# Kernel tuning notes

Hardware: AMD Instinct MI355X
Metric: run time of the kernel (lower is better)

## Reference

```python
import jax, jax.numpy as jnp
import numpy as np
from jax import lax

# ---- static config (matches init_kwargs) ----
B, D, H, HD, MLP = 64, 768, 12, 64, 3072
DEPTH = 11                     # trunk blocks; block 12 is used (twice) as b1/b2
IMG_H, IMG_W, P, S = 256, 128, 16, 12
NY, NX = (IMG_H - P) // S + 1, (IMG_W - P) // S + 1   # 21, 10
NP = NY * NX                   # 210 patches
N = NP + 1                     # +CLS = 211 tokens
NUM_CIDS = 8
SCALE = HD ** -0.5
SIE = 3.0                      # sie_xishu
SHIFT, GROUPS, DIV = 5, 2, 4
EPS = 1e-6
_PNAMES = ["ln1_g", "ln1_b", "qkv_w", "qkv_b", "proj_w", "proj_b",
           "ln2_g", "ln2_b", "fc1_w", "fc1_b", "fc2_w", "fc2_b"]


def layernorm(x, g, b):
    m = jnp.mean(x, -1, keepdims=True)
    v = jnp.mean(jnp.square(x - m), -1, keepdims=True)
    return (x - m) * lax.rsqrt(v + EPS) * g + b


def block(x, p):
    """Pre-norm ViT block: manual attention (q@k.T softmax @v) + GELU MLP."""
    ln1g, ln1b, qkvw, qkvb, projw, projb, ln2g, ln2b, fc1w, fc1b, fc2w, fc2b = p
    Bn, Nn = x.shape[0], x.shape[1]
    h = layernorm(x, ln1g, ln1b)
    qkv = (h @ qkvw + qkvb).reshape(Bn, Nn, 3, H, HD)
    q, k, v = qkv[:, :, 0], qkv[:, :, 1], qkv[:, :, 2]           # [B,N,H,HD]
    attn = jax.nn.softmax(jnp.einsum('bnhd,bmhd->bhnm', q * SCALE, k), axis=-1)
    o = jnp.einsum('bhnm,bmhd->bnhd', attn, v).reshape(Bn, Nn, D)
    x = x + o @ projw + projb
    h = layernorm(x, ln2g, ln2b)
    return x + jax.nn.gelu(h @ fc1w + fc1b, approximate=False) @ fc2w + fc2b


def _block_params(k, lead=()):
    ks = jax.random.split(k, 4)
    z = lambda s: jnp.zeros(lead + s, jnp.float32)
    o = lambda s: jnp.ones(lead + s, jnp.float32)
    r = lambda kk, s, fan: jax.random.normal(kk, lead + s, jnp.float32) * (fan ** -0.5)
    return dict(ln1_g=o((D,)), ln1_b=z((D,)),
                qkv_w=r(ks[0], (D, 3 * D), D), qkv_b=z((3 * D,)),
                proj_w=r(ks[1], (D, D), D), proj_b=z((D,)),
                ln2_g=o((D,)), ln2_b=z((D,)),
                fc1_w=r(ks[2], (D, MLP), D), fc1_b=z((MLP,)),
                fc2_w=r(ks[3], (MLP, D), MLP), fc2_b=z((D,)))


def setup_inputs() -> dict:
    key = jax.random.key(0)
    k = jax.random.split(key, 8)
    inp = {
        "x": jax.random.normal(k[0], (B, 3, IMG_H, IMG_W), jnp.float32),
        "cids": jax.random.randint(k[1], (B,), 0, NUM_CIDS),
        "conv_w": jax.random.normal(k[2], (D, 3, P, P), jnp.float32) * np.float32(np.sqrt(2.0 / (P * P * D))),
        "conv_b": jnp.zeros((D,), jnp.float32),
        "cls_token": jax.random.normal(k[3], (1, 1, D), jnp.float32) * 0.02,
        "pos_embed": jax.random.normal(k[4], (1, N, D), jnp.float32) * 0.02,
        "sie_embed": jax.random.normal(k[5], (NUM_CIDS, 1, D), jnp.float32) * 0.02,
    }
    for name, arr in _block_params(k[6], (DEPTH,)).items():
        inp["blk_" + name] = arr
    for pre, kk in (("b1_", jax.random.fold_in(key, 101)), ("b2_", jax.random.fold_in(key, 102))):
        for name, arr in _block_params(kk).items():
            inp[pre + name] = arr
        inp[pre + "norm_g"] = jnp.ones((D,), jnp.float32)
        inp[pre + "norm_b"] = jnp.zeros((D,), jnp.float32)
    return inp


def reference(x, cids, conv_w, conv_b, cls_token, pos_embed, sie_embed,
              blk_ln1_g, blk_ln1_b, blk_qkv_w, blk_qkv_b, blk_proj_w, blk_proj_b,
              blk_ln2_g, blk_ln2_b, blk_fc1_w, blk_fc1_b, blk_fc2_w, blk_fc2_b,
              b1_ln1_g, b1_ln1_b, b1_qkv_w, b1_qkv_b, b1_proj_w, b1_proj_b,
              b1_ln2_g, b1_ln2_b, b1_fc1_w, b1_fc1_b, b1_fc2_w, b1_fc2_b,
              b1_norm_g, b1_norm_b,
              b2_ln1_g, b2_ln1_b, b2_qkv_w, b2_qkv_b, b2_proj_w, b2_proj_b,
              b2_ln2_g, b2_ln2_b, b2_fc1_w, b2_fc1_b, b2_fc2_w, b2_fc2_b,
              b2_norm_g, b2_norm_b):
    Bn = x.shape[0]
    # overlapping patch embed: Conv2d(3->768, k=16, s=12), flatten, transpose
    y = lax.conv_general_dilated(x, conv_w, (S, S), 'VALID',
                                 dimension_numbers=('NCHW', 'OIHW', 'NCHW'))
    y = (y + conv_b[None, :, None, None]).reshape(Bn, D, NP).transpose(0, 2, 1)
    t = jnp.concatenate([jnp.broadcast_to(cls_token, (Bn, 1, D)), y], axis=1)
    t = t + pos_embed + SIE * sie_embed[cids]   # SIE camera embedding
    # 11 trunk blocks via scan over stacked params
    stk = (blk_ln1_g, blk_ln1_b, blk_qkv_w, blk_qkv_b, blk_proj_w, blk_proj_b,
           blk_ln2_g, blk_ln2_b, blk_fc1_w, blk_fc1_b, blk_fc2_w, blk_fc2_b)
    t = lax.scan(lambda c, p: (block(c, p), None), t, stk)[0]
    # global branch: b1 = block12 + final norm, take CLS
    b1p = (b1_ln1_g, b1_ln1_b, b1_qkv_w, b1_qkv_b, b1_proj_w, b1_proj_b,
           b1_ln2_g, b1_ln2_b, b1_fc1_w, b1_fc1_b, b1_fc2_w, b1_fc2_b)
    f0 = layernorm(block(t, b1p), b1_norm_g, b1_norm_b)[:, 0]
    # shuffle_unit(t, shift=5, group=2, begin=1) -> jigsaw rearranged patches [B,210,D]
    xs = jnp.concatenate([t[:, SHIFT:], t[:, 1:SHIFT]], axis=1)
    xs = xs.reshape(Bn, GROUPS, -1, D).transpose(0, 2, 1, 3).reshape(Bn, -1, D)
    token = t[:, 0:1]
    pl = NP // DIV                                   # 52
    b2p = (b2_ln1_g, b2_ln1_b, b2_qkv_w, b2_qkv_b, b2_proj_w, b2_proj_b,
           b2_ln2_g, b2_ln2_b, b2_fc1_w, b2_fc1_b, b2_fc2_w, b2_fc2_b)
    feats = [f0]
    for i in range(DIV):
        seg = jnp.concatenate([token, xs[:, i * pl:(i + 1) * pl]], axis=1)   # [B,53,D]
        feats.append(layernorm(block(seg, b2p), b2_norm_g, b2_norm_b)[:, 0])
    # eval output with neck_feat='before': necks pass features through;
    # concat global + local/divide_length -> [B, 5*768]
    return jnp.concatenate([feats[0]] + [f / DIV for f in feats[1:]], axis=1)
```

## Files before the change

kernel.cpp:

```cpp
#include <hip/hip_runtime.h>
#include <hip/hip_bf16.h>
#include <cstdint>
#include <cstddef>
#include <math.h>

using bf16 = __hip_bfloat16;
typedef __bf16 bf16x8 __attribute__((ext_vector_type(8)));
typedef float f32x4 __attribute__((ext_vector_type(4)));

static constexpr int NHEAD = 12;
static constexpr int NTOK  = 211;
static constexpr int DEPTH = 11;

static __device__ __forceinline__ void gload_lds16(const bf16* g, bf16* lds) {
  __builtin_amdgcn_global_load_lds(
      (const __attribute__((address_space(1))) uint32_t*)g,
      (__attribute__((address_space(3))) uint32_t*)lds,
      16, 0, 0);
}

__device__ __forceinline__ float gelu_f(float x) {
  float u = x * (0.7978845608f + 0.0356774081f * x * x);
  float t = 1.f - 2.f / (__expf(2.f * u) + 1.f);
  return 0.5f * x * (1.f + t);
}

static __device__ __forceinline__ unsigned short bf16_bits(float x) {
  return __builtin_bit_cast(unsigned short, __float2bfloat16(x));
}

template <bool GELU, bool RES, typename CT>
__global__ __launch_bounds__(256) void gemm_db(
    const bf16* __restrict__ A, const bf16* __restrict__ Bt,
    const float* __restrict__ bias, const float* __restrict__ res,
    CT* __restrict__ C, int M, int N, int K, int gn, int sA, int sR, int sC)
{
  __shared__ bf16 sb[2][8192];

  const int tid = threadIdx.x;
  const int w = tid >> 6, l = tid & 63;
  const int lr = l & 15, lg = l >> 4;
  const int wr = (w >> 1) * 64, wc = (w & 1) * 64;

  const int nwg = gridDim.x, lin = blockIdx.x;
  const int q = nwg >> 3, r = nwg & 7;
  const int xcd = lin & 7, pos = lin >> 3;
  const int wg = (xcd < r ? xcd * (q + 1) : r * (q + 1) + (xcd - r) * q) + pos;
  const int bm0 = (wg / gn) * 128, bn0 = (wg % gn) * 128;

  f32x4 acc[4][4];
#pragma unroll
  for (int i = 0; i < 4; ++i)
#pragma unroll
    for (int j = 0; j < 4; ++j) acc[i][j] = f32x4{0.f, 0.f, 0.f, 0.f};

  size_t aof[2], bof[2]; int dst[2];
#pragma unroll
  for (int j = 0; j < 2; ++j) {
    const int c = j * 256 + tid;
    const int row = c >> 2;
    const int ch = (c & 3) ^ ((row >> 1) & 3);
    int ar = bm0 + row; if (ar >= M) ar = M - 1;
    aof[j] = (size_t)ar * sA + ch * 8;
    bof[j] = (size_t)(bn0 + row) * K + ch * 8;
    dst[j] = c * 8;
  }

  const int nt = K >> 5;

  auto stage = [&](int t) {
    bf16* s = sb[t & 1];
    const size_t ko = (size_t)t * 32;
    gload_lds16(A + aof[0] + ko, s + dst[0]);
    gload_lds16(A + aof[1] + ko, s + dst[1]);
    gload_lds16(Bt + bof[0] + ko, s + 4096 + dst[0]);
    gload_lds16(Bt + bof[1] + ko, s + 4096 + dst[1]);
  };

  stage(0);
  __syncthreads();

  const int swz = (lg ^ ((lr >> 1) & 3)) * 8;

  for (int t = 0; t < nt; ++t) {
    if (t + 1 < nt) stage(t + 1);
    const bf16* As = sb[t & 1];
    const bf16* Bs = As + 4096;
    bf16x8 af[4], bv[4];
#pragma unroll
    for (int mi = 0; mi < 4; ++mi)
      af[mi] = *(const bf16x8*)(As + (wr + mi * 16 + lr) * 32 + swz);
#pragma unroll
    for (int ni = 0; ni < 4; ++ni)
      bv[ni] = *(const bf16x8*)(Bs + (wc + ni * 16 + lr) * 32 + swz);
#pragma unroll
    for (int mi = 0; mi < 4; ++mi)
#pragma unroll
      for (int ni = 0; ni < 4; ++ni)
        acc[mi][ni] = __builtin_amdgcn_mfma_f32_16x16x32_bf16(af[mi], bv[ni], acc[mi][ni], 0, 0, 0);
    __syncthreads();
  }

  if constexpr (sizeof(CT) == 2) {
    char* lb = (char*)sb;
#pragma unroll
    for (int mi = 0; mi < 4; ++mi) {
#pragma unroll
      for (int ni = 0; ni < 4; ++ni) {
        const int cloc = wc + ni * 16 + lr;
        const float bvl = bias[bn0 + cloc];
#pragma unroll
        for (int r2 = 0; r2 < 4; ++r2) {
          const int rowl = wr + mi * 16 + lg * 4 + r2;
          float v = acc[mi][ni][r2] + bvl;
          if constexpr (GELU) v = gelu_f(v);
          *(unsigned short*)(lb + rowl * 256 + ((cloc * 2) ^ (((rowl >> 1) & 6) << 4))) =
              bf16_bits(v);
        }
      }
    }
    __syncthreads();
#pragma unroll
    for (int j = 0; j < 8; ++j) {
      const int flat = j * 256 + tid;
      const int row = flat >> 4, ch = flat & 15;
      const int grow = bm0 + row;
      if (grow < M) {
        const f32x4 v = *(const f32x4*)(lb + row * 256 + ((ch * 16) ^ (((row >> 1) & 6) << 4)));
        *(f32x4*)((char*)C + ((size_t)grow * sC + bn0 + ch * 8) * 2) = v;
      }
    }
  } else {
#pragma unroll
    for (int mi = 0; mi < 4; ++mi) {
#pragma unroll
      for (int ni = 0; ni < 4; ++ni) {
        const int col = bn0 + wc + ni * 16 + lr;
        const float bvl = bias[col];
#pragma unroll
        for (int r2 = 0; r2 < 4; ++r2) {
          const int row = bm0 + wr + mi * 16 + lg * 4 + r2;
          if (row < M) {
            float v = acc[mi][ni][r2] + bvl;
            if constexpr (GELU) v = gelu_f(v);
            if constexpr (RES) v += res[(size_t)row * sR + col];
            C[(size_t)row * sC + col] = v;
          }
        }
      }
    }
  }
}

__global__ __launch_bounds__(256) void vtrans_kernel(
    const bf16* __restrict__ qkv, bf16* __restrict__ vT, int ntok, int pad)
{
  __shared__ unsigned short t[224 * 65];
  const int bb = blockIdx.x, h = blockIdx.y;
  const unsigned short* src = (const unsigned short*)qkv + (size_t)bb * ntok * 2304 + 1536 + h * 64;
  for (int idx = threadIdx.x; idx < ntok * 64; idx += 256) {
    int tok = idx >> 6, d = idx & 63;
    t[tok * 65 + d] = src[(size_t)tok * 2304 + d];
  }
  __syncthreads();
  unsigned short* dst = (unsigned short*)vT + (size_t)(bb * 12 + h) * 64 * pad;
  for (int idx = threadIdx.x; idx < 64 * ntok; idx += 256) {
    int d = idx / ntok, tok = idx - d * ntok;
    dst[(size_t)d * pad + tok] = t[tok * 65 + d];
  }
}

template <int NKF, bool ONLY0>
__global__ __launch_bounds__(256) void attn_kernel(
    const bf16* __restrict__ qkv, const bf16* __restrict__ vT,
    bf16* __restrict__ ao, int ntok, int pad)
{
  constexpr int NPAD = NKF * 16;
  __shared__ bf16 Pl[4][16][NPAD];
  const int bb = blockIdx.x;
  const int h = blockIdx.y;
  const int tid = threadIdx.x;
  const int w = tid >> 6, l = tid & 63;
  const int lr = l & 15, lg = l >> 4;
  if (ONLY0 && w > 0) return;
  const __bf16* base = reinterpret_cast<const __bf16*>(qkv) + (size_t)bb * ntok * 2304 + h * 64;
  const __bf16* vt = reinterpret_cast<const __bf16*>(vT) + (size_t)(bb * 12 + h) * 64 * pad;

  for (int qt = w; qt < (ONLY0 ? 1 : NKF); qt += 4) {
    int qrow = qt * 16 + lr; if (qrow >= ntok) qrow = ntok - 1;
    const __bf16* qp = base + (size_t)qrow * 2304 + lg * 8;
    const bf16x8 qf0 = *reinterpret_cast<const bf16x8*>(qp);
    const bf16x8 qf1 = *reinterpret_cast<const bf16x8*>(qp + 32);

    f32x4 s[NKF];
#pragma unroll
    for (int kf = 0; kf < NKF; ++kf) {
      int krow = kf * 16 + lr; if (krow >= ntok) krow = ntok - 1;
      const __bf16* kp = base + (size_t)krow * 2304 + 768 + lg * 8;
      f32x4 a = f32x4{0.f, 0.f, 0.f, 0.f};
      a = __builtin_amdgcn_mfma_f32_16x16x32_bf16(qf0, *reinterpret_cast<const bf16x8*>(kp), a, 0, 0, 0);
      a = __builtin_amdgcn_mfma_f32_16x16x32_bf16(qf1, *reinterpret_cast<const bf16x8*>(kp + 32), a, 0, 0, 0);
      s[kf] = a;
    }

    float rs[4];
#pragma unroll
    for (int r = 0; r < 4; ++r) {
      float mx = -1e30f;
#pragma unroll
      for (int kf = 0; kf < NKF; ++kf)
        if (kf * 16 + lr < ntok) mx = fmaxf(mx, s[kf][r]);
#pragma unroll
      for (int d = 1; d < 16; d <<= 1) mx = fmaxf(mx, __shfl_xor(mx, d));
      float sum = 0.f;
#pragma unroll
      for (int kf = 0; kf < NKF; ++kf) {
        float p = 0.f;
        if (kf * 16 + lr < ntok) p = __expf((s[kf][r] - mx) * 0.125f);
        sum += p;
        Pl[w][lg * 4 + r][kf * 16 + lr] = __float2bfloat16(p);
      }
#pragma unroll
      for (int d = 1; d < 16; d <<= 1) sum += __shfl_xor(sum, d);
      rs[r] = sum;
    }
    __builtin_amdgcn_s_waitcnt(0);

    f32x4 o[4];
#pragma unroll
    for (int ni = 0; ni < 4; ++ni) o[ni] = f32x4{0.f, 0.f, 0.f, 0.f};
#pragma unroll
    for (int ks = 0; ks < NPAD / 32; ++ks) {
      const bf16x8 pa = *reinterpret_cast<const bf16x8*>(&Pl[w][lr][ks * 32 + lg * 8]);
#pragma unroll
      for (int ni = 0; ni < 4; ++ni) {
        const bf16x8 vb = *reinterpret_cast<const bf16x8*>(
            vt + (size_t)(ni * 16 + lr) * pad + ks * 32 + lg * 8);
        o[ni] = __builtin_amdgcn_mfma_f32_16x16x32_bf16(pa, vb, o[ni], 0, 0, 0);
      }
    }
#pragma unroll
    for (int ni = 0; ni < 4; ++ni)
#pragma unroll
      for (int r = 0; r < 4; ++r) {
        int qq = qt * 16 + lg * 4 + r;
        if (qq < (ONLY0 ? 1 : ntok)) {
          float val = o[ni][r] / rs[r];
          ao[((size_t)bb * ntok + qq) * 768 + h * 64 + ni * 16 + lr] = __float2bfloat16(val);
        }
      }
  }
}

static __device__ __forceinline__ void ln_row(
    const float* __restrict__ x, const float* __restrict__ g, const float* __restrict__ b,
    bf16* __restrict__ out, int row, int l)
{
  const float4* xr = reinterpret_cast<const float4*>(x + (size_t)row * 768);
  float4 v[3]; float s = 0.f;
#pragma unroll
  for (int i = 0; i < 3; ++i) {
    v[i] = xr[l + i * 64];
    s += v[i].x + v[i].y + v[i].z + v[i].w;
  }
#pragma unroll
  for (int d = 1; d < 64; d <<= 1) s += __shfl_xor(s, d);
  float mean = s * (1.f / 768.f);
  float s2 = 0.f;
#pragma unroll
  for (int i = 0; i < 3; ++i) {
    float a0 = v[i].x - mean, a1 = v[i].y - mean, a2 = v[i].z - mean, a3 = v[i].w - mean;
    s2 += a0 * a0 + a1 * a1 + a2 * a2 + a3 * a3;
  }
#pragma unroll
  for (int d = 1; d < 64; d <<= 1) s2 += __shfl_xor(s2, d);
  float rstd = rsqrtf(s2 * (1.f / 768.f) + 1e-6f);
  const float4* g4 = reinterpret_cast<const float4*>(g);
  const float4* b4 = reinterpret_cast<const float4*>(b);
  unsigned short* orow = reinterpret_cast<unsigned short*>(out + (size_t)row * 768);
#pragma unroll
  for (int i = 0; i < 3; ++i) {
    float4 gg = g4[l + i * 64], bb = b4[l + i * 64];
    ushort4 pk;
    pk.x = bf16_bits((v[i].x - mean) * rstd * gg.x + bb.x);
    pk.y = bf16_bits((v[i].y - mean) * rstd * gg.y + bb.y);
    pk.z = bf16_bits((v[i].z - mean) * rstd * gg.z + bb.z);
    pk.w = bf16_bits((v[i].w - mean) * rstd * gg.w + bb.w);
    *reinterpret_cast<ushort4*>(orow + (l + i * 64) * 4) = pk;
  }
}

__global__ __launch_bounds__(256) void ln_kernel(
    const float* __restrict__ x, const float* __restrict__ g, const float* __restrict__ b,
    bf16* __restrict__ out, int Mrows)
{
  int row = blockIdx.x * 4 + (threadIdx.x >> 6);
  if (row >= Mrows) return;
  ln_row(x, g, b, out, row, threadIdx.x & 63);
}

__global__ __launch_bounds__(256) void tln_kernel(
    const float* __restrict__ w0, const float* __restrict__ w1,
    const float* __restrict__ w2, const float* __restrict__ w3,
    bf16* __restrict__ d0, bf16* __restrict__ d1,
    bf16* __restrict__ d2, bf16* __restrict__ d3,
    const float* __restrict__ x, const float* __restrict__ g,
    const float* __restrict__ b, bf16* __restrict__ outh, int Mrows)
{
  __shared__ float tile[32][33];
  int id = blockIdx.x;
  if (id >= 6912) {
    int row = (id - 6912) * 4 + (threadIdx.x >> 6);
    if (row < Mrows) ln_row(x, g, b, outh, row, threadIdx.x & 63);
    return;
  }
  const float* in; bf16* out; int R, C, tt;
  if (id < 1728)      { in = w0; out = d0; R = 768;  C = 2304; tt = id; }
  else if (id < 2304) { in = w1; out = d1; R = 768;  C = 768;  tt = id - 1728; }
  else if (id < 4608) { in = w2; out = d2; R = 768;  C = 3072; tt = id - 2304; }
  else                { in = w3; out = d3; R = 3072; C = 768;  tt = id - 4608; }
  const int tc = C >> 5;
  int c0 = (tt % tc) * 32, r0 = (tt / tc) * 32;
  int tx = threadIdx.x & 31, ty = threadIdx.x >> 5;
#pragma unroll
  for (int i = 0; i < 4; ++i) {
    int rr = ty + i * 8;
    tile[rr][tx] = in[(size_t)(r0 + rr) * C + c0 + tx];
  }
  __syncthreads();
#pragma unroll
  for (int i = 0; i < 4; ++i) {
    int c = ty + i * 8;
    out[(size_t)(c0 + c) * R + r0 + tx] = __float2bfloat16(tile[tx][c]);
  }
}

__global__ __launch_bounds__(256) void ln_head_kernel(
    const float* __restrict__ x, int tokstride, const float* __restrict__ g,
    const float* __restrict__ b, float* __restrict__ out, int nbb, int mode)
{
  int bb = blockIdx.x * 4 + (threadIdx.x >> 6);
  if (bb >= nbb) return;
  int l = threadIdx.x & 63;
  const float* xr = x + (size_t)bb * tokstride * 768;
  float v[12]; float s = 0.f;
#pragma unroll
  for (int i = 0; i < 12; ++i) { v[i] = xr[l + i * 64]; s += v[i]; }
#pragma unroll
  for (int d = 1; d < 64; d <<= 1) s += __shfl_xor(s, d);
  float mean = s * (1.f / 768.f);
  float s2 = 0.f;
#pragma unroll
  for (int i = 0; i < 12; ++i) { float t = v[i] - mean; s2 += t * t; }
#pragma unroll
  for (int d = 1; d < 64; d <<= 1) s2 += __shfl_xor(s2, d);
  float rstd = rsqrtf(s2 * (1.f / 768.f) + 1e-6f);
  float scale = mode ? 0.25f : 1.f;
  int b_ = mode ? (bb & 63) : bb;
  int off = mode ? (1 + (bb >> 6)) * 768 : 0;
  float* orow = out + (size_t)b_ * 3840 + off;
#pragma unroll
  for (int i = 0; i < 12; ++i) {
    orow[l + i * 64] = ((v[i] - mean) * rstd * g[l + i * 64] + b[l + i * 64]) * scale;
  }
}

__global__ void prep_kernel(const float* __restrict__ x, bf16* __restrict__ pm,
                            const float* __restrict__ convw, bf16* __restrict__ cw)
{
  int idx = blockIdx.x * 256 + threadIdx.x;
  if (idx < 13440 * 768) {
    int k = idx % 768;
    int m = idx / 768;
    int b = m / 210, p = m % 210;
    int py = p / 10, px = p % 10;
    int c = k >> 8, ij = k & 255, i = ij >> 4, j = ij & 15;
    pm[idx] = __float2bfloat16(x[(((size_t)b * 3 + c) * 256 + py * 12 + i) * 128 + px * 12 + j]);
  } else {
    int idx2 = idx - 13440 * 768;
    if (idx2 < 768 * 768) cw[idx2] = __float2bfloat16(convw[idx2]);
  }
}

__global__ void assemble_kernel(
    const bf16* __restrict__ y, const float* __restrict__ cls, const float* __restrict__ pos,
    const float* __restrict__ sie, const int* __restrict__ cids, float* __restrict__ tA)
{
  int idx = blockIdx.x * 256 + threadIdx.x;
  if (idx >= 13504 * 768) return;
  int d = idx % 768;
  int t = (idx / 768) % 211;
  int b = idx / (768 * 211);
  float v = pos[t * 768 + d] + 3.0f * sie[cids[b] * 768 + d];
  if (t == 0) v += cls[d];
  else v += __bfloat162float(y[((size_t)b * 210 + (t - 1)) * 768 + d]);
  tA[idx] = v;
}

__global__ void gather_kernel(const float* __restrict__ tA, float* __restrict__ tB)
{
  int idx = blockIdx.x * 256 + threadIdx.x;
  if (idx >= 256 * 53 * 768) return;
  int d = idx % 768;
  int jj = (idx / 768) % 53;
  int bb = idx / (768 * 53);
  int i = bb >> 6, b = bb & 63;
  int src;
  if (jj == 0) src = 0;
  else {
    int jx = i * 52 + (jj - 1);
    int mm = (jx & 1) * 105 + (jx >> 1);
    src = (mm < 206) ? (5 + mm) : (1 + (mm - 206));
  }
  tB[idx] = tA[((size_t)b * 211 + src) * 768 + d];
}

struct BlkP {
  const float *ln1_g, *ln1_b, *qkv_w, *qkv_b, *proj_w, *proj_b;
  const float *ln2_g, *ln2_b, *fc1_w, *fc1_b, *fc2_w, *fc2_b;
};

extern "C" void kernel_launch(void* const* d_in, const int* in_sizes, int n_in,
                              void* d_out, int out_size, void* d_ws, size_t ws_size,
                              hipStream_t stream)
{
  (void)in_sizes; (void)n_in; (void)out_size; (void)ws_size;
  const float* xin   = (const float*)d_in[0];
  const int*   cids  = (const int*)  d_in[1];
  const float* convw = (const float*)d_in[2];
  const float* convb = (const float*)d_in[3];
  const float* cls   = (const float*)d_in[4];
  const float* pos   = (const float*)d_in[5];
  const float* sie   = (const float*)d_in[6];
  float* out = (float*)d_out;

  char* ws = (char*)d_ws;
  bf16*  qkvT = (bf16*)(ws + 0);
  bf16*  projT = (bf16*)(ws + 3538944);
  bf16*  fc1T = (bf16*)(ws + 4718592);
  bf16*  fc2T = (bf16*)(ws + 9437184);
  float* tA   = (float*)(ws + 14155776);
  float* tB   = (float*)(ws + 55640064);
  bf16*  hb   = (bf16*)(ws + 97320960);
  bf16*  big  = (bf16*)(ws + 118161408);
  bf16*  ao   = (bf16*)(ws + 201523200);
  bf16*  vTb  = (bf16*)(ws + 222363648);
  char*  sbuf = ws + 118161408 + 73400320;
  float* y0   = (float*)(sbuf);
  bf16*  hb0  = (bf16*)(sbuf + 786432);
  bf16*  big0 = (bf16*)(sbuf + 1179648);
  float* f0b  = (float*)(sbuf + 2752512);

  dim3 blk(256);

  auto apply_block = [&](float* xbuf, const BlkP& p, int nb, int ntok_) {
    const int M = nb * ntok_;
    const int gm = (M + 127) / 128;
    const int pad = (ntok_ == NTOK) ? 224 : 64;
    tln_kernel<<<dim3(6912 + (M + 3) / 4), blk, 0, stream>>>(
        p.qkv_w, p.proj_w, p.fc1_w, p.fc2_w, qkvT, projT, fc1T, fc2T,
        xbuf, p.ln1_g, p.ln1_b, hb, M);
    gemm_db<false, false, bf16><<<dim3(gm * 18), blk, 0, stream>>>(
        hb, qkvT, p.qkv_b, nullptr, big, M, 2304, 768, 18, 768, 2304, 2304);
    vtrans_kernel<<<dim3(nb, NHEAD), blk, 0, stream>>>(big, vTb, ntok_, pad);
    attn_kernel<14, false><<<dim3(nb, NHEAD), blk, 0, stream>>>(big, vTb, ao, ntok_, pad);
    gemm_db<false, true, float><<<dim3(gm * 6), blk, 0, stream>>>(
        ao, projT, p.proj_b, xbuf, xbuf, M, 768, 768, 6, 768, 768, 768);
    ln_kernel<<<dim3((M + 3) / 4), blk, 0, stream>>>(xbuf, p.ln2_g, p.ln2_b, hb, M);
    gemm_db<true, false, bf16><<<dim3(gm * 24), blk, 0, stream>>>(
        hb, fc1T, p.fc1_b, nullptr, big, M, 3072, 768, 24, 768, 3072, 3072);
    gemm_db<false, true, float><<<dim3(gm * 6), blk, 0, stream>>>(
        big, fc2T, p.fc2_b, xbuf, xbuf, M, 768, 3072, 6, 3072, 768, 768);
  };

  auto apply_head_block = [&](const float* xsrc, const BlkP& p, int nb, int ntok_,
                              const float* ng, const float* nbias, int mode) {
    const int M = nb * ntok_;
    const int gm = (M + 127) / 128;
    const int gm0 = (nb + 127) / 128;
    const int pad = (ntok_ == NTOK) ? 224 : 64;
    const int ts = ntok_ * 768;
    tln_kernel<<<dim3(6912 + (M + 3) / 4), blk, 0, stream>>>(
        p.qkv_w, p.proj_w, p.fc1_w, p.fc2_w, qkvT, projT, fc1T, fc2T,
        xsrc, p.ln1_g, p.ln1_b, hb, M);
    gemm_db<false, false, bf16><<<dim3(gm * 12), blk, 0, stream>>>(
        hb, qkvT + 768 * 768, p.qkv_b + 768, nullptr, big + 768,
        M, 1536, 768, 12, 768, 0, 2304);
    gemm_db<false, false, bf16><<<dim3(gm0 * 6), blk, 0, stream>>>(
        hb, qkvT, p.qkv_b, nullptr, big,
        nb, 768, 768, 6, ntok_ * 768, 0, ntok_ * 2304);
    vtrans_kernel<<<dim3(nb, NHEAD), blk, 0, stream>>>(big, vTb, ntok_, pad);
    if (ntok_ == NTOK)
      attn_kernel<14, true><<<dim3(nb, NHEAD), blk, 0, stream>>>(big, vTb, ao, ntok_, pad);
    else
      attn_kernel<4, true><<<dim3(nb, NHEAD), blk, 0, stream>>>(big, vTb, ao, ntok_, pad);
    gemm_db<false, true, float><<<dim3(gm0 * 6), blk, 0, stream>>>(
        ao, projT, p.proj_b, xsrc, y0, nb, 768, 768, 6, ts, ts, 768);
    ln_kernel<<<dim3((nb + 3) / 4), blk, 0, stream>>>(y0, p.ln2_g, p.ln2_b, hb0, nb);
    gemm_db<true, false, bf16><<<dim3(gm0 * 24), blk, 0, stream>>>(
        hb0, fc1T, p.fc1_b, nullptr, big0, nb, 3072, 768, 24, 768, 3072, 3072);
    gemm_db<false, true, float><<<dim3(gm0 * 6), blk, 0, stream>>>(
        big0, fc2T, p.fc2_b, y0, f0b, nb, 768, 3072, 6, 3072, 768, 768);
    ln_head_kernel<<<dim3((nb + 3) / 4), blk, 0, stream>>>(
        f0b, 1, ng, nbias, out, nb, mode);
  };

  {
    int total = 13440 * 768 + 768 * 768;
    prep_kernel<<<dim3((total + 255) / 256), blk, 0, stream>>>(xin, big, convw, qkvT);
    gemm_db<false, false, bf16><<<dim3(105 * 6), blk, 0, stream>>>(
        big, qkvT, convb, nullptr, ao, 13440, 768, 768, 6, 768, 768, 768);
    total = 13504 * 768;
    assemble_kernel<<<dim3((total + 255) / 256), blk, 0, stream>>>(ao, cls, pos, sie, cids, tA);
  }

  const float* bp[12];
  for (int i = 0; i < 12; ++i) bp[i] = (const float*)d_in[7 + i];
  for (int dd = 0; dd < DEPTH; ++dd) {
    BlkP p;
    p.ln1_g = bp[0] + dd * 768;                p.ln1_b = bp[1] + dd * 768;
    p.qkv_w = bp[2] + (size_t)dd * 768 * 2304; p.qkv_b = bp[3] + dd * 2304;
    p.proj_w = bp[4] + (size_t)dd * 768 * 768; p.proj_b = bp[5] + dd * 768;
    p.ln2_g = bp[6] + dd * 768;                p.ln2_b = bp[7] + dd * 768;
    p.fc1_w = bp[8] + (size_t)dd * 768 * 3072; p.fc1_b = bp[9] + dd * 3072;
    p.fc2_w = bp[10] + (size_t)dd * 3072 * 768; p.fc2_b = bp[11] + dd * 768;
    apply_block(tA, p, 64, NTOK);
  }

  {
    BlkP p;
    p.ln1_g = (const float*)d_in[19]; p.ln1_b = (const float*)d_in[20];
    p.qkv_w = (const float*)d_in[21]; p.qkv_b = (const float*)d_in[22];
    p.proj_w = (const float*)d_in[23]; p.proj_b = (const float*)d_in[24];
    p.ln2_g = (const float*)d_in[25]; p.ln2_b = (const float*)d_in[26];
    p.fc1_w = (const float*)d_in[27]; p.fc1_b = (const float*)d_in[28];
    p.fc2_w = (const float*)d_in[29]; p.fc2_b = (const float*)d_in[30];
    apply_head_block(tA, p, 64, NTOK,
                     (const float*)d_in[31], (const float*)d_in[32], 0);
  }

  {
    int total = 256 * 53 * 768;
    gather_kernel<<<dim3((total + 255) / 256), blk, 0, stream>>>(tA, tB);
    BlkP p;
    p.ln1_g = (const float*)d_in[33]; p.ln1_b = (const float*)d_in[34];
    p.qkv_w = (const float*)d_in[35]; p.qkv_b = (const float*)d_in[36];
    p.proj_w = (const float*)d_in[37]; p.proj_b = (const float*)d_in[38];
    p.ln2_g = (const float*)d_in[39]; p.ln2_b = (const float*)d_in[40];
    p.fc1_w = (const float*)d_in[41]; p.fc1_b = (const float*)d_in[42];
    p.fc2_w = (const float*)d_in[43]; p.fc2_b = (const float*)d_in[44];
    apply_head_block(tB, p, 256, 53,
                     (const float*)d_in[45], (const float*)d_in[46], 1);
  }
}
```

Before: 5.102 ms.

## Scatter QKV GEMM output into per-head contiguous Q/K/V buffers

The QKV GEMM epilogue now writes Q, K and V directly into head-major [batch*head, pad, 64] buffers instead of an interleaved [tokens, 2304] matrix. The attention kernel and the V-transpose kernel read these contiguous per-head tiles, which avoids strided 4.6KB-row gathers. The cost is extra index math in the epilogue and a rearranged workspace layout whose buffers may overlap.

Result: no change. 5.088 ms (-0.3%).

```diff
diff --git a/kernel.cpp b/kernel.cpp
--- a/kernel.cpp
+++ b/kernel.cpp
@@ -29,11 +29,13 @@
   return __builtin_bit_cast(unsigned short, __float2bfloat16(x));
 }
 
-template <bool GELU, bool RES, typename CT>
+template <bool GELU, bool RES, typename CT, int OUT>
 __global__ __launch_bounds__(256) void gemm_db(
     const bf16* __restrict__ A, const bf16* __restrict__ Bt,
     const float* __restrict__ bias, const float* __restrict__ res,
-    CT* __restrict__ C, int M, int N, int K, int gn, int sA, int sR, int sC)
+    CT* __restrict__ C, int M, int N, int K, int gn, int sA, int sR, int sC,
+    bf16* __restrict__ qh, bf16* __restrict__ kh, bf16* __restrict__ vh,
+    int pad, int ntd, int coff)
 {
   __shared__ bf16 sb[2][8192];
 
@@ -101,7 +103,7 @@
     __syncthreads();
   }
 
-  if constexpr (sizeof(CT) == 2) {
+  if constexpr (OUT == 2 || sizeof(CT) == 2) {
     char* lb = (char*)sb;
 #pragma unroll
     for (int mi = 0; mi < 4; ++mi) {
@@ -127,7 +129,18 @@
       const int grow = bm0 + row;
       if (grow < M) {
         const f32x4 v = *(const f32x4*)(lb + row * 256 + ((ch * 16) ^ (((row >> 1) & 6) << 4)));
-        *(f32x4*)((char*)C + ((size_t)grow * sC + bn0 + ch * 8) * 2) = v;
+        if constexpr (OUT == 2) {
+          const int col0 = bn0 + ch * 8 + coff;
+          const int region = (col0 >= 1536) ? 2 : (col0 >= 768 ? 1 : 0);
+          const int c7 = col0 - region * 768;
+          const int h = c7 >> 6, d = c7 & 63;
+          const int bb2 = grow / ntd;
+          const int tok = grow - bb2 * ntd;
+          bf16* db = (region == 0) ? qh : ((region == 1) ? kh : vh);
+          *(f32x4*)((char*)db + (((size_t)(bb2 * 12 + h) * pad + tok) * 64 + d) * 2) = v;
+        } else {
+          *(f32x4*)((char*)C + ((size_t)grow * sC + bn0 + ch * 8) * 2) = v;
+        }
       }
     }
   } else {
@@ -153,27 +166,27 @@
 }
 
 __global__ __launch_bounds__(256) void vtrans_kernel(
-    const bf16* __restrict__ qkv, bf16* __restrict__ vT, int ntok, int pad)
+    const bf16* __restrict__ vcomp, bf16* __restrict__ vT, int ntok, int pad)
 {
   __shared__ unsigned short t[224 * 65];
   const int bb = blockIdx.x, h = blockIdx.y;
-  const unsigned short* src = (const unsigned short*)qkv + (size_t)bb * ntok * 2304 + 1536 + h * 64;
+  const unsigned short* src = (const unsigned short*)vcomp + (size_t)(bb * 12 + h) * pad * 64;
   for (int idx = threadIdx.x; idx < ntok * 64; idx += 256) {
     int tok = idx >> 6, d = idx & 63;
-    t[tok * 65 + d] = src[(size_t)tok * 2304 + d];
+    t[tok * 65 + d] = src[idx];
   }
   __syncthreads();
-  unsigned short* dst = (unsigned short*)vT + (size_t)(bb * 12 + h) * 64 * pad;
+  unsigned short* dstp = (unsigned short*)vT + (size_t)(bb * 12 + h) * 64 * pad;
   for (int idx = threadIdx.x; idx < 64 * ntok; idx += 256) {
     int d = idx / ntok, tok = idx - d * ntok;
-    dst[(size_t)d * pad + tok] = t[tok * 65 + d];
+    dstp[(size_t)d * pad + tok] = t[tok * 65 + d];
   }
 }
 
 template <int NKF, bool ONLY0>
 __global__ __launch_bounds__(256) void attn_kernel(
-    const bf16* __restrict__ qkv, const bf16* __restrict__ vT,
-    bf16* __restrict__ ao, int ntok, int pad)
+    const bf16* __restrict__ qb, const bf16* __restrict__ kb,
+    const bf16* __restrict__ vT, bf16* __restrict__ ao, int ntok, int pad)
 {
   constexpr int NPAD = NKF * 16;
   __shared__ bf16 Pl[4][16][NPAD];
@@ -183,12 +196,14 @@
   const int w = tid >> 6, l = tid & 63;
   const int lr = l & 15, lg = l >> 4;
   if (ONLY0 && w > 0) return;
-  const __bf16* base = reinterpret_cast<const __bf16*>(qkv) + (size_t)bb * ntok * 2304 + h * 64;
-  const __bf16* vt = reinterpret_cast<const __bf16*>(vT) + (size_t)(bb * 12 + h) * 64 * pad;
+  const int bbh = bb * 12 + h;
+  const __bf16* qbase = reinterpret_cast<const __bf16*>(qb) + (size_t)bbh * pad * 64;
+  const __bf16* kbase = reinterpret_cast<const __bf16*>(kb) + (size_t)bbh * pad * 64;
+  const __bf16* vt = reinterpret_cast<const __bf16*>(vT) + (size_t)bbh * 64 * pad;
 
   for (int qt = w; qt < (ONLY0 ? 1 : NKF); qt += 4) {
     int qrow = qt * 16 + lr; if (qrow >= ntok) qrow = ntok - 1;
-    const __bf16* qp = base + (size_t)qrow * 2304 + lg * 8;
+    const __bf16* qp = qbase + qrow * 64 + lg * 8;
     const bf16x8 qf0 = *reinterpret_cast<const bf16x8*>(qp);
     const bf16x8 qf1 = *reinterpret_cast<const bf16x8*>(qp + 32);
 
@@ -196,7 +211,7 @@
 #pragma unroll
     for (int kf = 0; kf < NKF; ++kf) {
       int krow = kf * 16 + lr; if (krow >= ntok) krow = ntok - 1;
-      const __bf16* kp = base + (size_t)krow * 2304 + 768 + lg * 8;
+      const __bf16* kp = kbase + krow * 64 + lg * 8;
       f32x4 a = f32x4{0.f, 0.f, 0.f, 0.f};
       a = __builtin_amdgcn_mfma_f32_16x16x32_bf16(qf0, *reinterpret_cast<const bf16x8*>(kp), a, 0, 0, 0);
       a = __builtin_amdgcn_mfma_f32_16x16x32_bf16(qf1, *reinterpret_cast<const bf16x8*>(kp + 32), a, 0, 0, 0);
@@ -442,14 +457,17 @@
   float* tA   = (float*)(ws + 14155776);
   float* tB   = (float*)(ws + 55640064);
   bf16*  hb   = (bf16*)(ws + 97320960);
+  bf16*  qb   = (bf16*)(ws + 118161408);
+  bf16*  kb   = (bf16*)(ws + 143327232);
+  bf16*  vb   = (bf16*)(ws + 168493056);
   bf16*  big  = (bf16*)(ws + 118161408);
-  bf16*  ao   = (bf16*)(ws + 201523200);
-  bf16*  vTb  = (bf16*)(ws + 222363648);
-  char*  sbuf = ws + 118161408 + 73400320;
+  char*  sbuf = ws + 193658880;
   float* y0   = (float*)(sbuf);
   bf16*  hb0  = (bf16*)(sbuf + 786432);
   bf16*  big0 = (bf16*)(sbuf + 1179648);
   float* f0b  = (float*)(sbuf + 2752512);
+  bf16*  ao   = (bf16*)(ws + 201523200);
+  bf16*  vTb  = (bf16*)(ws + 222363648);
 
   dim3 blk(256);
 
@@ -460,17 +478,21 @@
     tln_kernel<<<dim3(6912 + (M + 3) / 4), blk, 0, stream>>>(
         p.qkv_w, p.proj_w, p.fc1_w, p.fc2_w, qkvT, projT, fc1T, fc2T,
         xbuf, p.ln1_g, p.ln1_b, hb, M);
-    gemm_db<false, false, bf16><<<dim3(gm * 18), blk, 0, stream>>>(
-        hb, qkvT, p.qkv_b, nullptr, big, M, 2304, 768, 18, 768, 2304, 2304);
-    vtrans_kernel<<<dim3(nb, NHEAD), blk, 0, stream>>>(big, vTb, ntok_, pad);
-    attn_kernel<14, false><<<dim3(nb, NHEAD), blk, 0, stream>>>(big, vTb, ao, ntok_, pad);
-    gemm_db<false, true, float><<<dim3(gm * 6), blk, 0, stream>>>(
-        ao, projT, p.proj_b, xbuf, xbuf, M, 768, 768, 6, 768, 768, 768);
+    gemm_db<false, false, bf16, 2><<<dim3(gm * 18), blk, 0, stream>>>(
+        hb, qkvT, p.qkv_b, nullptr, (bf16*)nullptr, M, 2304, 768, 18, 768, 0, 0,
+        qb, kb, vb, pad, ntok_, 0);
+    vtrans_kernel<<<dim3(nb, NHEAD), blk, 0, stream>>>(vb, vTb, ntok_, pad);
+    attn_kernel<14, false><<<dim3(nb, NHEAD), blk, 0, stream>>>(qb, kb, vTb, ao, ntok_, pad);
+    gemm_db<false, true, float, 0><<<dim3(gm * 6), blk, 0, stream>>>(
+        ao, projT, p.proj_b, xbuf, xbuf, M, 768, 768, 6, 768, 768, 768,
+        nullptr, nullptr, nullptr, 0, 1, 0);
     ln_kernel<<<dim3((M + 3) / 4), blk, 0, stream>>>(xbuf, p.ln2_g, p.ln2_b, hb, M);
-    gemm_db<true, false, bf16><<<dim3(gm * 24), blk, 0, stream>>>(
-        hb, fc1T, p.fc1_b, nullptr, big, M, 3072, 768, 24, 768, 3072, 3072);
-    gemm_db<false, true, float><<<dim3(gm * 6), blk, 0, stream>>>(
-        big, fc2T, p.fc2_b, xbuf, xbuf, M, 768, 3072, 6, 3072, 768, 768);
+    gemm_db<true, false, bf16, 0><<<dim3(gm * 24), blk, 0, stream>>>(
+        hb, fc1T, p.fc1_b, nullptr, big, M, 3072, 768, 24, 768, 3072, 3072,
+        nullptr, nullptr, nullptr, 0, 1, 0);
+    gemm_db<false, true, float, 0><<<dim3(gm * 6), blk, 0, stream>>>(
+        big, fc2T, p.fc2_b, xbuf, xbuf, M, 768, 3072, 6, 3072, 768, 768,
+        nullptr, nullptr, nullptr, 0, 1, 0);
   };
 
   auto apply_head_block = [&](const float* xsrc, const BlkP& p, int nb, int ntok_,
@@ -483,24 +505,27 @@
     tln_kernel<<<dim3(6912 + (M + 3) / 4), blk, 0, stream>>>(
         p.qkv_w, p.proj_w, p.fc1_w, p.fc2_w, qkvT, projT, fc1T, fc2T,
         xsrc, p.ln1_g, p.ln1_b, hb, M);
-    gemm_db<false, false, bf16><<<dim3(gm * 12), blk, 0, stream>>>(
-        hb, qkvT + 768 * 768, p.qkv_b + 768, nullptr, big + 768,
-        M, 1536, 768, 12, 768, 0, 2304);
-    gemm_db<false, false, bf16><<<dim3(gm0 * 6), blk, 0, stream>>>(
-        hb, qkvT, p.qkv_b, nullptr, big,
-        nb, 768, 768, 6, ntok_ * 768, 0, ntok_ * 2304);
-    vtrans_kernel<<<dim3(nb, NHEAD), blk, 0, stream>>>(big, vTb, ntok_, pad);
+    gemm_db<false, false, bf16, 2><<<dim3(gm * 12), blk, 0, stream>>>(
+        hb, qkvT + 768 * 768, p.qkv_b + 768, nullptr, (bf16*)nullptr,
+        M, 1536, 768, 12, 768, 0, 0, qb, kb, vb, pad, ntok_, 768);
+    gemm_db<false, false, bf16, 2><<<dim3(gm0 * 6), blk, 0, stream>>>(
+        hb, qkvT, p.qkv_b, nullptr, (bf16*)nullptr,
+        nb, 768, 768, 6, ntok_ * 768, 0, 0, qb, kb, vb, pad, 1, 0);
+    vtrans_kernel<<<dim3(nb, NHEAD), blk, 0, stream>>>(vb, vTb, ntok_, pad);
     if (ntok_ == NTOK)
-      attn_kernel<14, true><<<dim3(nb, NHEAD), blk, 0, stream>>>(big, vTb, ao, ntok_, pad);
+      attn_kernel<14, true><<<dim3(nb, NHEAD), blk, 0, stream>>>(qb, kb, vTb, ao, ntok_, pad);
     else
-      attn_kernel<4, true><<<dim3(nb, NHEAD), blk, 0, stream>>>(big, vTb, ao, ntok_, pad);
-    gemm_db<false, true, float><<<dim3(gm0 * 6), blk, 0, stream>>>(
-        ao, projT, p.proj_b, xsrc, y0, nb, 768, 768, 6, ts, ts, 768);
+      attn_kernel<4, true><<<dim3(nb, NHEAD), blk, 0, stream>>>(qb, kb, vTb, ao, ntok_, pad);
+    gemm_db<false, true, float, 0><<<dim3(gm0 * 6), blk, 0, stream>>>(
+        ao, projT, p.proj_b, xsrc, y0, nb, 768, 768, 6, ts, ts, 768,
+        nullptr, nullptr, nullptr, 0, 1, 0);
     ln_kernel<<<dim3((nb + 3) / 4), blk, 0, stream>>>(y0, p.ln2_g, p.ln2_b, hb0, nb);
-    gemm_db<true, false, bf16><<<dim3(gm0 * 24), blk, 0, stream>>>(
-        hb0, fc1T, p.fc1_b, nullptr, big0, nb, 3072, 768, 24, 768, 3072, 3072);
-    gemm_db<false, true, float><<<dim3(gm0 * 6), blk, 0, stream>>>(
-        big0, fc2T, p.fc2_b, y0, f0b, nb, 768, 3072, 6, 3072, 768, 768);
+    gemm_db<true, false, bf16, 0><<<dim3(gm0 * 24), blk, 0, stream>>>(
+        hb0, fc1T, p.fc1_b, nullptr, big0, nb, 3072, 768, 24, 768, 3072, 3072,
+        nullptr, nullptr, nullptr, 0, 1, 0);
+    gemm_db<false, true, float, 0><<<dim3(gm0 * 6), blk, 0, stream>>>(
+        big0, fc2T, p.fc2_b, y0, f0b, nb, 768, 3072, 6, 3072, 768, 768,
+        nullptr, nullptr, nullptr, 0, 1, 0);
     ln_head_kernel<<<dim3((nb + 3) / 4), blk, 0, stream>>>(
         f0b, 1, ng, nbias, out, nb, mode);
   };
@@ -508,8 +533,9 @@
   {
     int total = 13440 * 768 + 768 * 768;
     prep_kernel<<<dim3((total + 255) / 256), blk, 0, stream>>>(xin, big, convw, qkvT);
-    gemm_db<false, false, bf16><<<dim3(105 * 6), blk, 0, stream>>>(
-        big, qkvT, convb, nullptr, ao, 13440, 768, 768, 6, 768, 768, 768);
+    gemm_db<false, false, bf16, 0><<<dim3(105 * 6), blk, 0, stream>>>(
+        big, qkvT, convb, nullptr, ao, 13440, 768, 768, 6, 768, 768, 768,
+        nullptr, nullptr, nullptr, 0, 1, 0);
     total = 13504 * 768;
     assemble_kernel<<<dim3((total + 255) / 256), blk, 0, stream>>>(ao, cls, pos, sie, cids, tA);
   }
```
